# Kernel tuning notes

Measured on AMD Instinct MI355X. Metric: run time of the kernel, lower is better.

## Reference

```python
import jax, jax.numpy as jnp
import numpy as np

B = 8
D = 512        # d_hidn
H = 8          # n_head
DH = 64        # d_head
L = 6          # n_layer
DFF = 2048     # d_ff
GRID = 10
DMLP = 1024
NOUT = 1
EPS = 1e-6
CIN = 2048
SEQ = 1 + 24 * 32 + 9 * 12 + 5 * 7  # 912


def setup_inputs() -> dict:
    key = jax.random.key(0)
    ks = jax.random.split(key, 40)
    rn = lambda k, s, sc=0.02: jax.random.normal(k, s, jnp.float32) * sc
    inp = {
        "feat_dis_org": jax.random.normal(ks[0], (B, CIN, 24, 32), jnp.float32),
        "feat_dis_ref_1": jax.random.normal(ks[1], (B, CIN, 9, 12), jnp.float32),
        "feat_dis_ref_2": jax.random.normal(ks[2], (B, CIN, 5, 7), jnp.float32),
        "conv_w": rn(ks[3], (D, CIN)),
        "conv_b": rn(ks[4], (D,)),
        "scale_org_emb": jax.random.uniform(ks[5], (D,), jnp.float32),
        "ref_1_emb": jax.random.uniform(ks[6], (D,), jnp.float32),
        "ref_2_emb": rn(ks[7], (D,), 1.0),
        "pos_emb": rn(ks[8], (GRID, GRID, D), 0.02),
        "cls_token": rn(ks[9], (D,), 0.02),
        "Wq": rn(ks[10], (L, D, D)), "bq": rn(ks[11], (L, D)),
        "Wk": rn(ks[12], (L, D, D)), "bk": rn(ks[13], (L, D)),
        "Wv": rn(ks[14], (L, D, D)), "bv": rn(ks[15], (L, D)),
        "Wo": rn(ks[16], (L, D, D)), "bo": rn(ks[17], (L, D)),
        "ln1_g": jnp.ones((L, D), jnp.float32), "ln1_b": jnp.zeros((L, D), jnp.float32),
        "w1": rn(ks[18], (L, DFF, D)), "b1": rn(ks[19], (L, DFF)),
        "w2": rn(ks[20], (L, D, DFF)), "b2": rn(ks[21], (L, D)),
        "ln2_g": jnp.ones((L, D), jnp.float32), "ln2_b": jnp.zeros((L, D), jnp.float32),
        "proj_w1": rn(ks[22], (DMLP, D)),
        "proj_w2": rn(ks[23], (NOUT, DMLP)),
        "mask_inputs": jnp.ones((B, SEQ), jnp.int32),
    }
    return inp


def _ln(x, g, b):
    m = jnp.mean(x, -1, keepdims=True)
    v = jnp.mean((x - m) ** 2, -1, keepdims=True)
    return (x - m) * jax.lax.rsqrt(v + EPS) * g + b


def _embed(feat, chan_emb, conv_w, conv_b, pos_emb):
    # 1x1 conv (conv_enc) as a channel contraction: [b,2048,h,w] -> [b,D,h,w]
    x = jnp.einsum('bchw,dc->bdhw', feat, conv_w) + conv_b[None, :, None, None]
    x = x + chan_emb[None, :, None, None]           # scale/ref embedding
    h, w = x.shape[2], x.shape[3]
    # vectorized version of the nested-loop gather: t_i = int(i/h*Grid)
    ti = (jnp.arange(h) * GRID) // h
    tj = (jnp.arange(w) * GRID) // w
    sp = pos_emb[ti][:, tj]                          # [h,w,D]
    x = x + jnp.transpose(sp, (2, 0, 1))[None]       # [b,D,h,w]
    return jnp.transpose(x.reshape(x.shape[0], D, h * w), (0, 2, 1))  # [b,hw,D]


def reference(feat_dis_org, feat_dis_ref_1, feat_dis_ref_2, conv_w, conv_b,
              scale_org_emb, ref_1_emb, ref_2_emb, pos_emb, cls_token,
              Wq, bq, Wk, bk, Wv, bv, Wo, bo, ln1_g, ln1_b,
              w1, b1, w2, b2, ln2_g, ln2_b, proj_w1, proj_w2, mask_inputs):
    t_org = _embed(feat_dis_org, scale_org_emb, conv_w, conv_b, pos_emb)
    t_r1 = _embed(feat_dis_ref_1, ref_1_emb, conv_w, conv_b, pos_emb)
    t_r2 = _embed(feat_dis_ref_2, ref_2_emb, conv_w, conv_b, pos_emb)
    cls = jnp.broadcast_to(cls_token[None, None, :], (B, 1, D))
    x = jnp.concatenate([cls, t_org, t_r1, t_r2], axis=1)   # [B,SEQ,D]

    pad = (mask_inputs == 0)[:, None, None, :]              # [B,1,1,SEQ]
    scale = 1.0 / (DH ** 0.5)

    for i in range(L):
        s = x.shape[1]
        q = (x @ Wq[i].T + bq[i]).reshape(B, s, H, DH).transpose(0, 2, 1, 3)
        k = (x @ Wk[i].T + bk[i]).reshape(B, s, H, DH).transpose(0, 2, 1, 3)
        v = (x @ Wv[i].T + bv[i]).reshape(B, s, H, DH).transpose(0, 2, 1, 3)
        scores = jnp.einsum('bhqd,bhkd->bhqk', q, k) * scale
        scores = jnp.where(pad, -1e9, scores)
        prob = jax.nn.softmax(scores, axis=-1)
        ctx = jnp.einsum('bhqk,bhkd->bhqd', prob, v)
        ctx = ctx.transpose(0, 2, 1, 3).reshape(B, s, H * DH)
        att = ctx @ Wo[i].T + bo[i]
        x = _ln(x + att, ln1_g[i], ln1_b[i])
        ff = jax.nn.gelu(x @ w1[i].T + b1[i], approximate=False) @ w2[i].T + b2[i]
        x = _ln(x + ff, ln2_g[i], ln2_b[i])

    cls_out = x[:, 0, :]
    hmlp = jax.nn.gelu(cls_out @ proj_w1.T, approximate=False)
    pred = hmlp @ proj_w2.T                                   # [B,1]
    return pred
```

## Files before the change

### kernel.cpp

```cpp
#include <hip/hip_runtime.h>
#include <hip/hip_bf16.h>
#include <math.h>

#define SEQ 912
#define NTOK 911
#define CIN_ 2048
#define NLAYER 6

typedef _Float16 f16x8 __attribute__((ext_vector_type(8)));
typedef _Float16 f16x4 __attribute__((ext_vector_type(4)));
typedef float f32x4 __attribute__((ext_vector_type(4)));

__device__ __forceinline__ float gelu_f(float x) {
    return 0.5f * x * (1.0f + erff(x * 0.70710678118654752f));
}

__device__ __forceinline__ int xcd_swizzle(int orig, int nwg) {
    int q = nwg >> 3, r = nwg & 7;
    int xcd = orig & 7, idx = orig >> 3;
    int base = (xcd < r) ? xcd * (q + 1) : r * (q + 1) + (xcd - r) * q;
    return base + idx;
}

__device__ __forceinline__ void gld16(const _Float16* g, _Float16* l) {
    __builtin_amdgcn_global_load_lds(
        (const __attribute__((address_space(1))) unsigned int*)g,
        (__attribute__((address_space(3))) unsigned int*)l,
        16, 0, 0);
}

__device__ __forceinline__ void stage_tile_g(const _Float16* Ab, const _Float16* Bb,
                                             size_t seg, _Float16* ldsW, int kk) {
    gld16(Ab + kk, ldsW);
    gld16(Ab + seg + kk, ldsW + 2048);
    gld16(Bb + kk, ldsW + 4096);
    gld16(Bb + seg + kk, ldsW + 6144);
}

__device__ __forceinline__ void compute_step_g(const _Float16* sb, int r0, int c0,
                                               int ln15, int quad, f32x4 (&acc)[4][4]) {
    f16x8 a[4], b[4];
#pragma unroll
    for (int i = 0; i < 4; ++i)
        a[i] = *(const f16x8*)&sb[(r0 + i * 16 + ln15) * 32 + quad * 8];
#pragma unroll
    for (int j = 0; j < 4; ++j)
        b[j] = *(const f16x8*)&sb[4096 + (c0 + j * 16 + ln15) * 32 + quad * 8];
#pragma unroll
    for (int i = 0; i < 4; ++i)
#pragma unroll
        for (int j = 0; j < 4; ++j)
            acc[i][j] = __builtin_amdgcn_mfma_f32_16x16x32_f16(a[i], b[j], acc[i][j], 0, 0, 0);
}

template <int ACT, int QKV>
__global__ __launch_bounds__(256) void gemm16(
    const _Float16* __restrict__ A, const _Float16* __restrict__ B,
    const float* __restrict__ bias, _Float16* __restrict__ Cout,
    _Float16* __restrict__ vT, int M, int N, int K, int ldc)
{
    __shared__ __align__(16) _Float16 smem[2 * 8192];
    _Float16* Cs = smem;
    const int t = threadIdx.x;
    const int nbx = N >> 7;
    const int swz = xcd_swizzle(blockIdx.x, gridDim.x);
    const int by = swz / nbx, bx = swz - by * nbx;
    const int m0 = by * 128, n0 = bx * 128;
    const int lane = t & 63, w = t >> 6;
    const int r0 = (w >> 1) * 64, c0 = (w & 1) * 64;
    const int ln15 = lane & 15, quad = lane >> 4;

    f32x4 zero = {0.f, 0.f, 0.f, 0.f};
    f32x4 acc[4][4];
#pragma unroll
    for (int i = 0; i < 4; ++i)
#pragma unroll
        for (int j = 0; j < 4; ++j) acc[i][j] = zero;

    const _Float16* Ab = A + (size_t)(m0 + w * 16 + (lane >> 2)) * K + (lane & 3) * 8;
    const _Float16* Bb = B + (size_t)(n0 + w * 16 + (lane >> 2)) * K + (lane & 3) * 8;
    const size_t seg = (size_t)64 * K;
    _Float16* ldsW = smem + w * 512;

    stage_tile_g(Ab, Bb, seg, ldsW, 0);
    __syncthreads();

    const int nK = K >> 5;
    for (int s = 0; s < nK; s += 2) {
        stage_tile_g(Ab, Bb, seg, ldsW + 8192, (s + 1) << 5);
        compute_step_g(smem, r0, c0, ln15, quad, acc);
        __syncthreads();
        if (s + 2 < nK) stage_tile_g(Ab, Bb, seg, ldsW, (s + 2) << 5);
        compute_step_g(smem + 8192, r0, c0, ln15, quad, acc);
        __syncthreads();
    }

    if (QKV && n0 >= 1024) {
#pragma unroll
        for (int j = 0; j < 4; ++j) {
            int gn = n0 + c0 + j * 16 + ln15;
            float bv = bias[gn];
            int chan = gn - 1024;
            int hh = chan >> 6, d = chan & 63;
#pragma unroll
            for (int i = 0; i < 4; ++i) {
                int gmBase = m0 + r0 + i * 16 + quad * 4;
                int bb = gmBase / 912, s = gmBase - bb * 912;
                f16x4 hv4;
#pragma unroll
                for (int r = 0; r < 4; ++r) hv4[r] = (_Float16)(acc[i][j][r] + bv);
                *(f16x4*)&vT[((size_t)((bb * 8 + hh) * 64 + d)) * 960 + s] = hv4;
            }
        }
    } else {
#pragma unroll
        for (int half = 0; half < 2; ++half) {
            if ((w >> 1) == half) {
#pragma unroll
                for (int j = 0; j < 4; ++j) {
                    float bv = bias[n0 + c0 + j * 16 + ln15];
#pragma unroll
                    for (int i = 0; i < 4; ++i)
#pragma unroll
                        for (int r = 0; r < 4; ++r) {
                            float val = acc[i][j][r] + bv;
                            if (ACT == 1) val = gelu_f(val);
                            Cs[(i * 16 + quad * 4 + r) * 136 + c0 + j * 16 + ln15] = (_Float16)val;
                        }
                }
            }
            __syncthreads();
#pragma unroll
            for (int uu = 0; uu < 4; ++uu) {
                int u = t + uu * 256;
                int lr = u >> 4, ch = (u & 15) * 8;
                int gm = m0 + half * 64 + lr;
                if (gm < M)
                    *(f16x8*)&Cout[(size_t)gm * ldc + n0 + ch] = *(const f16x8*)&Cs[lr * 136 + ch];
            }
            __syncthreads();
        }
    }
}

__device__ __forceinline__ void stage_tile_s(const _Float16* Ab, const _Float16* Bb,
                                             size_t seg, _Float16* ldsW, int kk) {
    gld16(Ab + kk, ldsW);
    gld16(Ab + seg + kk, ldsW + 2048);
    gld16(Bb + kk, ldsW + 4096);
}

__device__ __forceinline__ void compute_step_s(const _Float16* sb, int r0, int c0,
                                               int ln15, int quad, f32x4 (&acc)[4][2]) {
    f16x8 a[4], b[2];
#pragma unroll
    for (int i = 0; i < 4; ++i)
        a[i] = *(const f16x8*)&sb[(r0 + i * 16 + ln15) * 32 + quad * 8];
#pragma unroll
    for (int j = 0; j < 2; ++j)
        b[j] = *(const f16x8*)&sb[4096 + (c0 + j * 16 + ln15) * 32 + quad * 8];
#pragma unroll
    for (int i = 0; i < 4; ++i)
#pragma unroll
        for (int j = 0; j < 2; ++j)
            acc[i][j] = __builtin_amdgcn_mfma_f32_16x16x32_f16(a[i], b[j], acc[i][j], 0, 0, 0);
}

__global__ __launch_bounds__(256) void gemm16_splitk(
    const _Float16* __restrict__ A, const _Float16* __restrict__ B,
    float* __restrict__ part, int M, int N, int K)
{
    __shared__ __align__(16) _Float16 smem[2 * 6144];
    const int t = threadIdx.x;
    const int nbx = N >> 6;
    const int swz = xcd_swizzle(blockIdx.x, gridDim.x);
    const int by = swz / nbx, bx = swz - by * nbx;
    const int m0 = by * 128, n0 = bx * 64;
    const int z = blockIdx.z;
    const int lane = t & 63, w = t >> 6;
    const int r0 = (w >> 1) * 64, c0 = (w & 1) * 32;
    const int ln15 = lane & 15, quad = lane >> 4;
    const int Ks = K >> 1;
    const int kBeg = z * Ks;

    f32x4 zero = {0.f, 0.f, 0.f, 0.f};
    f32x4 acc[4][2];
#pragma unroll
    for (int i = 0; i < 4; ++i)
#pragma unroll
        for (int j = 0; j < 2; ++j) acc[i][j] = zero;

    const _Float16* Ab = A + (size_t)(m0 + w * 16 + (lane >> 2)) * K + kBeg + (lane & 3) * 8;
    const _Float16* Bb = B + (size_t)(n0 + w * 16 + (lane >> 2)) * K + kBeg + (lane & 3) * 8;
    const size_t seg = (size_t)64 * K;
    _Float16* ldsW = smem + w * 512;

    stage_tile_s(Ab, Bb, seg, ldsW, 0);
    __syncthreads();

    const int nK = Ks >> 5;
    for (int s = 0; s < nK; s += 2) {
        stage_tile_s(Ab, Bb, seg, ldsW + 6144, (s + 1) << 5);
        compute_step_s(smem, r0, c0, ln15, quad, acc);
        __syncthreads();
        if (s + 2 < nK) stage_tile_s(Ab, Bb, seg, ldsW, (s + 2) << 5);
        compute_step_s(smem + 6144, r0, c0, ln15, quad, acc);
        __syncthreads();
    }

    float* out = part + (size_t)z * M * N;
#pragma unroll
    for (int j = 0; j < 2; ++j) {
        int gn = n0 + c0 + j * 16 + ln15;
#pragma unroll
        for (int i = 0; i < 4; ++i) {
            int gmBase = m0 + r0 + i * 16 + quad * 4;
#pragma unroll
            for (int r = 0; r < 4; ++r) {
                int gm = gmBase + r;
                if (gm < M) out[(size_t)gm * N + gn] = acc[i][j][r];
            }
        }
    }
}

__global__ __launch_bounds__(256) void cast16_kernel(
    const float* __restrict__ src, _Float16* __restrict__ dst, int n4)
{
    int i = blockIdx.x * 256 + threadIdx.x;
    if (i < n4) {
        float4 v = ((const float4*)src)[i];
        f16x4 h;
        h[0] = (_Float16)v.x; h[1] = (_Float16)v.y;
        h[2] = (_Float16)v.z; h[3] = (_Float16)v.w;
        ((f16x4*)dst)[i] = h;
    }
}

__global__ __launch_bounds__(256) void cast2_kernel(
    const float* __restrict__ s1, _Float16* __restrict__ d1, int n4_1,
    const float* __restrict__ s2, _Float16* __restrict__ d2, int n4_2)
{
    int i = blockIdx.x * 256 + threadIdx.x;
    if (i < n4_1) {
        float4 v = ((const float4*)s1)[i];
        f16x4 h;
        h[0] = (_Float16)v.x; h[1] = (_Float16)v.y;
        h[2] = (_Float16)v.z; h[3] = (_Float16)v.w;
        ((f16x4*)d1)[i] = h;
    } else {
        int j = i - n4_1;
        if (j < n4_2) {
            float4 v = ((const float4*)s2)[j];
            f16x4 h;
            h[0] = (_Float16)v.x; h[1] = (_Float16)v.y;
            h[2] = (_Float16)v.z; h[3] = (_Float16)v.w;
            ((f16x4*)d2)[j] = h;
        }
    }
}

__global__ __launch_bounds__(256) void pack_qkvw_kernel(
    const float* __restrict__ Wq, const float* __restrict__ Wk,
    const float* __restrict__ Wv, _Float16* __restrict__ dst)
{
    int idx = blockIdx.x * 256 + threadIdx.x;
    if (idx >= 6 * 1536 * 128) return;
    int c4 = idx & 127;
    int rc = idx >> 7;
    int r = rc % 1536;
    int l = rc / 1536;
    const float* src = (r < 512) ? Wq : (r < 1024) ? Wk : Wv;
    float4 v = *(const float4*)(src + ((size_t)l * 512 + (r & 511)) * 512 + c4 * 4);
    f16x4 h;
    h[0] = (_Float16)v.x; h[1] = (_Float16)v.y;
    h[2] = (_Float16)v.z; h[3] = (_Float16)v.w;
    *(f16x4*)(dst + ((size_t)l * 1536 + r) * 512 + c4 * 4) = h;
}

__global__ __launch_bounds__(256) void pack_qkvb_kernel(
    const float* __restrict__ bq, const float* __restrict__ bk,
    const float* __restrict__ bv, float* __restrict__ dst)
{
    int idx = blockIdx.x * 256 + threadIdx.x;
    if (idx < 6 * 1536) {
        int r = idx % 1536, l = idx / 1536;
        const float* s = (r < 512) ? bq : (r < 1024) ? bk : bv;
        dst[idx] = s[l * 512 + (r & 511)];
    }
}

__global__ __launch_bounds__(256) void transpose_feat_kernel(
    const float* __restrict__ feat, _Float16* __restrict__ patch, int HW, int tok_off)
{
    __shared__ float tile[32][33];
    const int b = blockIdx.z;
    const int c0 = blockIdx.y * 32;
    const int p0 = blockIdx.x * 32;
    const int tx = threadIdx.x, ty = threadIdx.y;
#pragma unroll
    for (int i = 0; i < 4; ++i) {
        int c = c0 + ty + i * 8;
        int p = p0 + tx;
        tile[ty + i * 8][tx] = (p < HW) ? feat[((size_t)b * CIN_ + c) * HW + p] : 0.f;
    }
    __syncthreads();
#pragma unroll
    for (int i = 0; i < 4; ++i) {
        int p = p0 + ty + i * 8;
        int c = c0 + tx;
        if (p < HW)
            patch[((size_t)(b * NTOK + tok_off + p)) * CIN_ + c] = (_Float16)tile[tx][ty + i * 8];
    }
}

__global__ __launch_bounds__(128) void build_x_red(
    const float* __restrict__ part, const float* __restrict__ conv_b,
    const float* __restrict__ cls_token,
    const float* __restrict__ emb_org, const float* __restrict__ emb_r1,
    const float* __restrict__ emb_r2, const float* __restrict__ pos_emb,
    float* __restrict__ x, _Float16* __restrict__ x16)
{
    const size_t ESTR = (size_t)7288 * 512;
    const int row = blockIdx.x;
    const int b = row / SEQ;
    const int tt = row - b * SEQ;
    const int d4 = threadIdx.x;
    float4 o;
    if (tt == 0) {
        o = ((const float4*)cls_token)[d4];
    } else {
        int tp = tt - 1;
        const float* ce; int hh, ww, p;
        if (tp < 768)      { p = tp;       hh = 24; ww = 32; ce = emb_org; }
        else if (tp < 876) { p = tp - 768; hh = 9;  ww = 12; ce = emb_r1; }
        else               { p = tp - 876; hh = 5;  ww = 7;  ce = emb_r2; }
        int i = p / ww, j = p - i * ww;
        int ti = (i * 10) / hh, tj = (j * 10) / ww;
        size_t prow = (size_t)(b * NTOK + tp) * 512;
        float4 t0 = ((const float4*)(part + prow))[d4];
        float4 t1 = ((const float4*)(part + ESTR + prow))[d4];
        float4 cb = ((const float4*)conv_b)[d4];
        float4 cv = ((const float4*)ce)[d4];
        float4 pv = ((const float4*)(pos_emb + (size_t)(ti * 10 + tj) * 512))[d4];
        o.x = t0.x + t1.x + cb.x + cv.x + pv.x;
        o.y = t0.y + t1.y + cb.y + cv.y + pv.y;
        o.z = t0.z + t1.z + cb.z + cv.z + pv.z;
        o.w = t0.w + t1.w + cb.w + cv.w + pv.w;
    }
    ((float4*)(x + (size_t)row * 512))[d4] = o;
    f16x4 h;
    h[0] = (_Float16)o.x; h[1] = (_Float16)o.y;
    h[2] = (_Float16)o.z; h[3] = (_Float16)o.w;
    ((f16x4*)(x16 + (size_t)row * 512))[d4] = h;
}

__global__ __launch_bounds__(64) void ln_residual_red(
    float* __restrict__ x, _Float16* __restrict__ x16,
    const float* __restrict__ part, const float* __restrict__ bias,
    const float* __restrict__ g, const float* __restrict__ bta)
{
    const size_t LSTR = (size_t)7296 * 512;
    const int row = blockIdx.x;
    const int t = threadIdx.x;
    float4* xr = (float4*)(x + (size_t)row * 512);
    const float4* p0 = (const float4*)(part + (size_t)row * 512);
    const float4* p1 = (const float4*)(part + LSTR + (size_t)row * 512);
    const float4* bb = (const float4*)bias;
    float4 a0 = xr[t], a1 = xr[t + 64];
    float4 q0 = p0[t], q1 = p0[t + 64];
    float4 r0 = p1[t], r1 = p1[t + 64];
    float4 c0 = bb[t], c1 = bb[t + 64];
    a0.x += q0.x + r0.x + c0.x; a0.y += q0.y + r0.y + c0.y;
    a0.z += q0.z + r0.z + c0.z; a0.w += q0.w + r0.w + c0.w;
    a1.x += q1.x + r1.x + c1.x; a1.y += q1.y + r1.y + c1.y;
    a1.z += q1.z + r1.z + c1.z; a1.w += q1.w + r1.w + c1.w;
    float s = a0.x + a0.y + a0.z + a0.w + a1.x + a1.y + a1.z + a1.w;
#pragma unroll
    for (int o = 32; o; o >>= 1) s += __shfl_xor(s, o, 64);
    const float mean = s * (1.f / 512.f);
    float sq = 0.f;
    sq += (a0.x - mean) * (a0.x - mean); sq += (a0.y - mean) * (a0.y - mean);
    sq += (a0.z - mean) * (a0.z - mean); sq += (a0.w - mean) * (a0.w - mean);
    sq += (a1.x - mean) * (a1.x - mean); sq += (a1.y - mean) * (a1.y - mean);
    sq += (a1.z - mean) * (a1.z - mean); sq += (a1.w - mean) * (a1.w - mean);
#pragma unroll
    for (int o = 32; o; o >>= 1) sq += __shfl_xor(sq, o, 64);
    const float rstd = rsqrtf(sq * (1.f / 512.f) + 1e-6f);
    const float4 g0 = ((const float4*)g)[t], g1 = ((const float4*)g)[t + 64];
    const float4 e0 = ((const float4*)bta)[t], e1 = ((const float4*)bta)[t + 64];
    float4 o0, o1;
    o0.x = (a0.x - mean) * rstd * g0.x + e0.x;
    o0.y = (a0.y - mean) * rstd * g0.y + e0.y;
    o0.z = (a0.z - mean) * rstd * g0.z + e0.z;
    o0.w = (a0.w - mean) * rstd * g0.w + e0.w;
    o1.x = (a1.x - mean) * rstd * g1.x + e1.x;
    o1.y = (a1.y - mean) * rstd * g1.y + e1.y;
    o1.z = (a1.z - mean) * rstd * g1.z + e1.z;
    o1.w = (a1.w - mean) * rstd * g1.w + e1.w;
    xr[t] = o0; xr[t + 64] = o1;
    f16x4 h0, h1;
    h0[0] = (_Float16)o0.x; h0[1] = (_Float16)o0.y;
    h0[2] = (_Float16)o0.z; h0[3] = (_Float16)o0.w;
    h1[0] = (_Float16)o1.x; h1[1] = (_Float16)o1.y;
    h1[2] = (_Float16)o1.z; h1[3] = (_Float16)o1.w;
    f16x4* xh = (f16x4*)(x16 + (size_t)row * 512);
    xh[t] = h0; xh[t + 64] = h1;
}

__global__ __launch_bounds__(256) void attn_mfma(
    const _Float16* __restrict__ qk, const _Float16* __restrict__ vT,
    const int* __restrict__ mask, _Float16* __restrict__ ctx)
{
    __shared__ __align__(16) _Float16 Ks[64 * 72];
    __shared__ __align__(16) _Float16 VTs[64 * 72];
    __shared__ __align__(16) _Float16 Pw[4][16 * 72];
    __shared__ float biasS[64];
    const int swz = xcd_swizzle(blockIdx.x, 960);
    const int qt = swz % 15;
    const int hb = swz / 15;
    const int h = hb & 7, b = hb >> 3;
    const int q0 = qt * 64;
    const int t = threadIdx.x;
    const int wave = t >> 6, lane = t & 63;
    const int ln15 = lane & 15, quad = lane >> 4;
    const int qrow = q0 + wave * 16 + ln15;

    f16x8 qf[2];
#pragma unroll
    for (int ks = 0; ks < 2; ++ks) {
        f16x8 z = {0, 0, 0, 0, 0, 0, 0, 0};
        qf[ks] = (qrow < SEQ)
            ? *(const f16x8*)(qk + (size_t)(b * SEQ + qrow) * 1024 + h * 64 + ks * 32 + quad * 8)
            : z;
    }

    f32x4 oacc[4];
    f32x4 zero = {0.f, 0.f, 0.f, 0.f};
#pragma unroll
    for (int dj = 0; dj < 4; ++dj) oacc[dj] = zero;
    float m_i = -1e30f, l_i = 0.f;

    for (int kb = 0; kb < 960; kb += 64) {
#pragma unroll
        for (int i = 0; i < 2; ++i) {
            int u = t + i * 256;
            int r = u >> 3, ch = (u & 7) * 8;
            int kg = kb + r;
            f16x8 kvv = {0, 0, 0, 0, 0, 0, 0, 0};
            if (kg < SEQ) kvv = *(const f16x8*)(qk + (size_t)(b * SEQ + kg) * 1024 + 512 + h * 64 + ch);
            *(f16x8*)&Ks[r * 72 + ch] = kvv;
            f16x8 vv = {0, 0, 0, 0, 0, 0, 0, 0};
            if (kb + ch < SEQ)
                vv = *(const f16x8*)(vT + ((size_t)((b * 8 + h) * 64 + r)) * 960 + kb + ch);
            *(f16x8*)&VTs[r * 72 + ch] = vv;
        }
        if (t < 64) {
            int kg = kb + t;
            biasS[t] = (kg < SEQ) ? (mask[b * SEQ + kg] ? 0.f : -1e9f) : -2e9f;
        }
        __syncthreads();

        f32x4 st[4];
#pragma unroll
        for (int jj = 0; jj < 4; ++jj) st[jj] = zero;
#pragma unroll
        for (int jj = 0; jj < 4; ++jj)
#pragma unroll
            for (int ks = 0; ks < 2; ++ks) {
                f16x8 kf = *(const f16x8*)&Ks[(jj * 16 + ln15) * 72 + ks * 32 + quad * 8];
                st[jj] = __builtin_amdgcn_mfma_f32_16x16x32_f16(kf, qf[ks], st[jj], 0, 0, 0);
            }

        float p[4][4];
        float mloc = -3e38f;
#pragma unroll
        for (int jj = 0; jj < 4; ++jj) {
            f32x4 bfr = *(const f32x4*)&biasS[jj * 16 + quad * 4];
#pragma unroll
            for (int r = 0; r < 4; ++r) {
                float sv = st[jj][r] * 0.125f + bfr[r];
                p[jj][r] = sv;
                mloc = fmaxf(mloc, sv);
            }
        }
        mloc = fmaxf(mloc, __shfl_xor(mloc, 16, 64));
        mloc = fmaxf(mloc, __shfl_xor(mloc, 32, 64));
        float mnew = fmaxf(m_i, mloc);
        float alpha = __expf(m_i - mnew);
        m_i = mnew;
        float sloc = 0.f;
#pragma unroll
        for (int jj = 0; jj < 4; ++jj)
#pragma unroll
            for (int r = 0; r < 4; ++r) {
                p[jj][r] = __expf(p[jj][r] - mnew);
                sloc += p[jj][r];
            }
        sloc += __shfl_xor(sloc, 16, 64);
        sloc += __shfl_xor(sloc, 32, 64);
        l_i = l_i * alpha + sloc;

        float ar[4];
#pragma unroll
        for (int r = 0; r < 4; ++r) ar[r] = __shfl(alpha, quad * 4 + r, 64);
#pragma unroll
        for (int dj = 0; dj < 4; ++dj)
#pragma unroll
            for (int r = 0; r < 4; ++r) oacc[dj][r] *= ar[r];

        _Float16* pw = &Pw[wave][0];
#pragma unroll
        for (int jj = 0; jj < 4; ++jj)
#pragma unroll
            for (int r = 0; r < 4; ++r)
                pw[ln15 * 72 + jj * 16 + quad * 4 + r] = (_Float16)p[jj][r];
        f16x8 pf[2];
#pragma unroll
        for (int ks = 0; ks < 2; ++ks)
            pf[ks] = *(const f16x8*)&pw[ln15 * 72 + ks * 32 + quad * 8];

#pragma unroll
        for (int dj = 0; dj < 4; ++dj)
#pragma unroll
            for (int ks = 0; ks < 2; ++ks) {
                f16x8 vf = *(const f16x8*)&VTs[(dj * 16 + ln15) * 72 + ks * 32 + quad * 8];
                oacc[dj] = __builtin_amdgcn_mfma_f32_16x16x32_f16(pf[ks], vf, oacc[dj], 0, 0, 0);
            }
        __syncthreads();
    }

    float linv[4];
#pragma unroll
    for (int r = 0; r < 4; ++r) linv[r] = 1.f / __shfl(l_i, quad * 4 + r, 64);
#pragma unroll
    for (int dj = 0; dj < 4; ++dj)
#pragma unroll
        for (int r = 0; r < 4; ++r) {
            int row = q0 + wave * 16 + quad * 4 + r;
            if (row < SEQ)
                ctx[(size_t)(b * SEQ + row) * 512 + h * 64 + dj * 16 + ln15] =
                    (_Float16)(oacc[dj][r] * linv[r]);
        }
}

__global__ __launch_bounds__(64) void head1_kernel(
    const float* __restrict__ x, const float* __restrict__ w,
    float* __restrict__ hmlp)
{
    const int n = blockIdx.x & 1023;
    const int b = blockIdx.x >> 10;
    const int t = threadIdx.x;
    const float4* cls = (const float4*)(x + (size_t)b * SEQ * 512);
    const float4* wr = (const float4*)(w + (size_t)n * 512);
    float s = 0.f;
#pragma unroll
    for (int i = 0; i < 2; ++i) {
        float4 a = cls[t + i * 64], c = wr[t + i * 64];
        s += a.x * c.x + a.y * c.y + a.z * c.z + a.w * c.w;
    }
#pragma unroll
    for (int o = 32; o; o >>= 1) s += __shfl_xor(s, o, 64);
    if (t == 0) hmlp[b * 1024 + n] = gelu_f(s);
}

__global__ __launch_bounds__(256) void head2_kernel(
    const float* __restrict__ hmlp, const float* __restrict__ w,
    float* __restrict__ out)
{
    __shared__ float red[4];
    const int b = blockIdx.x;
    const int t = threadIdx.x;
    float s = 0.f;
    for (int i = t; i < 1024; i += 256) s += hmlp[b * 1024 + i] * w[i];
#pragma unroll
    for (int o = 32; o; o >>= 1) s += __shfl_xor(s, o, 64);
    if ((t & 63) == 0) red[t >> 6] = s;
    __syncthreads();
    if (t == 0) out[b] = red[0] + red[1] + red[2] + red[3];
}

extern "C" void kernel_launch(void* const* d_in, const int* in_sizes, int n_in,
                              void* d_out, int out_size, void* d_ws, size_t ws_size,
                              hipStream_t stream)
{
    const float* feat_org = (const float*)d_in[0];
    const float* feat_r1  = (const float*)d_in[1];
    const float* feat_r2  = (const float*)d_in[2];
    const float* conv_w   = (const float*)d_in[3];
    const float* conv_b   = (const float*)d_in[4];
    const float* emb_org  = (const float*)d_in[5];
    const float* emb_r1   = (const float*)d_in[6];
    const float* emb_r2   = (const float*)d_in[7];
    const float* pos_emb  = (const float*)d_in[8];
    const float* cls_tok  = (const float*)d_in[9];
    const float* Wq = (const float*)d_in[10];
    const float* bq = (const float*)d_in[11];
    const float* Wk = (const float*)d_in[12];
    const float* bk = (const float*)d_in[13];
    const float* Wv = (const float*)d_in[14];
    const float* bv = (const float*)d_in[15];
    const float* Wo = (const float*)d_in[16];
    const float* bo = (const float*)d_in[17];
    const float* ln1g = (const float*)d_in[18];
    const float* ln1b = (const float*)d_in[19];
    const float* w1 = (const float*)d_in[20];
    const float* b1 = (const float*)d_in[21];
    const float* w2 = (const float*)d_in[22];
    const float* b2 = (const float*)d_in[23];
    const float* ln2g = (const float*)d_in[24];
    const float* ln2b = (const float*)d_in[25];
    const float* pw1 = (const float*)d_in[26];
    const float* pw2 = (const float*)d_in[27];
    const int*   mask = (const int*)d_in[28];

    char* base = (char*)d_ws;
    _Float16* ffh16 = (_Float16*)base;
    _Float16* patch16 = ffh16;
    base += (size_t)7296 * 2048 * 2;
    float* x = (float*)base; base += (size_t)7296 * 512 * 4;
    _Float16* qk16 = (_Float16*)base; base += (size_t)7296 * 1024 * 2;
    _Float16* vT16 = (_Float16*)base; base += (size_t)8 * 8 * 64 * 960 * 2;
    _Float16* ctx16 = (_Float16*)base; base += (size_t)7296 * 512 * 2;
    _Float16* x16   = (_Float16*)base; base += (size_t)7296 * 512 * 2;
    _Float16* wqkv_all = (_Float16*)base; base += (size_t)6 * 1536 * 512 * 2;
    _Float16* wo_all   = (_Float16*)base; base += (size_t)6 * 512 * 512 * 2;
    _Float16* w1_l16   = (_Float16*)base; base += (size_t)2048 * 512 * 2;
    _Float16* w2_l16   = (_Float16*)base; base += (size_t)512 * 2048 * 2;
    float* bqkv_all = (float*)base; base += 6 * 1536 * 4;
    float* hmlp = (float*)base; base += 8 * 1024 * 4;

    float* partO = (float*)ffh16;
    float* partF = (float*)qk16;
    _Float16* convw16 = x16;

    dim3 tb(32, 8);
    hipLaunchKernelGGL(transpose_feat_kernel, dim3(24, 64, 8), tb, 0, stream,
                       feat_org, patch16, 768, 0);
    hipLaunchKernelGGL(transpose_feat_kernel, dim3(4, 64, 8), tb, 0, stream,
                       feat_r1, patch16, 108, 768);
    hipLaunchKernelGGL(transpose_feat_kernel, dim3(2, 64, 8), tb, 0, stream,
                       feat_r2, patch16, 35, 876);
    hipLaunchKernelGGL(cast16_kernel, dim3(1024), 256, 0, stream,
                       conv_w, convw16, 512 * 2048 / 4);
    hipLaunchKernelGGL(cast16_kernel, dim3(1536), 256, 0, stream,
                       Wo, wo_all, 6 * 512 * 512 / 4);
    hipLaunchKernelGGL(pack_qkvw_kernel, dim3(4608), 256, 0, stream,
                       Wq, Wk, Wv, wqkv_all);
    hipLaunchKernelGGL(pack_qkvb_kernel, dim3(36), 256, 0, stream,
                       bq, bk, bv, bqkv_all);

    hipLaunchKernelGGL(gemm16_splitk, dim3(456, 1, 2), 256, 0, stream,
                       patch16, convw16, partF, 7288, 512, 2048);
    hipLaunchKernelGGL(build_x_red, dim3(7296), 128, 0, stream,
                       partF, conv_b, cls_tok, emb_org, emb_r1, emb_r2, pos_emb, x, x16);

    for (int l = 0; l < NLAYER; ++l) {
        hipLaunchKernelGGL(cast2_kernel, dim3(2048), 256, 0, stream,
                           w1 + (size_t)l * 2048 * 512, w1_l16, 2048 * 512 / 4,
                           w2 + (size_t)l * 512 * 2048, w2_l16, 512 * 2048 / 4);
        hipLaunchKernelGGL((gemm16<0, 1>), dim3(684), 256, 0, stream,
                           x16, wqkv_all + (size_t)l * 1536 * 512, bqkv_all + l * 1536,
                           qk16, vT16, 7296, 1536, 512, 1024);
        hipLaunchKernelGGL(attn_mfma, dim3(960), 256, 0, stream,
                           qk16, vT16, mask, ctx16);
        hipLaunchKernelGGL(gemm16_splitk, dim3(456, 1, 2), 256, 0, stream,
                           ctx16, wo_all + (size_t)l * 512 * 512, partO, 7296, 512, 512);
        hipLaunchKernelGGL(ln_residual_red, dim3(7296), 64, 0, stream,
                           x, x16, partO, bo + l * 512, ln1g + l * 512, ln1b + l * 512);
        hipLaunchKernelGGL((gemm16<1, 0>), dim3(912), 256, 0, stream,
                           x16, w1_l16, b1 + l * 2048,
                           ffh16, (_Float16*)nullptr, 7296, 2048, 512, 2048);
        hipLaunchKernelGGL(gemm16_splitk, dim3(456, 1, 2), 256, 0, stream,
                           ffh16, w2_l16, partF, 7296, 512, 2048);
        hipLaunchKernelGGL(ln_residual_red, dim3(7296), 64, 0, stream,
                           x, x16, partF, b2 + l * 512, ln2g + l * 512, ln2b + l * 512);
    }

    hipLaunchKernelGGL(head1_kernel, dim3(8 * 1024), 64, 0, stream, x, pw1, hmlp);
    hipLaunchKernelGGL(head2_kernel, dim3(8), 256, 0, stream, hmlp, pw2, (float*)d_out);
}
```

Measured before the change: 1.375 ms.

## Deepen GEMM LDS pipeline to four stages with explicit vmcnt waits

Both the main fp16 GEMM and the split-K GEMM move from a double-buffered LDS loop with two full __syncthreads per pair of k-steps to a 4-slot ring that keeps two tiles in flight. Each step uses one s_barrier gated by a partial s_waitcnt vmcnt. The aim is to overlap global-to-LDS loads with MFMA compute more deeply and to cut barrier stalls. The cost is doubled LDS per block, which may lower occupancy. Correctness now depends on the exact count of outstanding vm operations that each stage issues.

```diff
diff --git a/kernel.cpp b/kernel.cpp
--- a/kernel.cpp
+++ b/kernel.cpp
@@ -59,7 +59,7 @@
     const float* __restrict__ bias, _Float16* __restrict__ Cout,
     _Float16* __restrict__ vT, int M, int N, int K, int ldc)
 {
-    __shared__ __align__(16) _Float16 smem[2 * 8192];
+    __shared__ __align__(16) _Float16 smem[4 * 8192];
     _Float16* Cs = smem;
     const int t = threadIdx.x;
     const int nbx = N >> 7;
@@ -82,18 +82,25 @@
     const size_t seg = (size_t)64 * K;
     _Float16* ldsW = smem + w * 512;
 
+    const int nK = K >> 5;
     stage_tile_g(Ab, Bb, seg, ldsW, 0);
-    __syncthreads();
-
-    const int nK = K >> 5;
-    for (int s = 0; s < nK; s += 2) {
-        stage_tile_g(Ab, Bb, seg, ldsW + 8192, (s + 1) << 5);
-        compute_step_g(smem, r0, c0, ln15, quad, acc);
-        __syncthreads();
-        if (s + 2 < nK) stage_tile_g(Ab, Bb, seg, ldsW, (s + 2) << 5);
-        compute_step_g(smem + 8192, r0, c0, ln15, quad, acc);
-        __syncthreads();
-    }
+    stage_tile_g(Ab, Bb, seg, ldsW + 8192, 32);
+
+    for (int s = 0; s < nK - 2; ++s) {
+        stage_tile_g(Ab, Bb, seg, ldsW + ((s + 2) & 3) * 8192, (s + 2) << 5);
+        asm volatile("s_waitcnt vmcnt(8)" ::: "memory");
+        __builtin_amdgcn_s_barrier();
+        __builtin_amdgcn_sched_barrier(0);
+        compute_step_g(smem + (s & 3) * 8192, r0, c0, ln15, quad, acc);
+    }
+    asm volatile("s_waitcnt vmcnt(4)" ::: "memory");
+    __builtin_amdgcn_s_barrier();
+    __builtin_amdgcn_sched_barrier(0);
+    compute_step_g(smem + ((nK - 2) & 3) * 8192, r0, c0, ln15, quad, acc);
+    asm volatile("s_waitcnt vmcnt(0)" ::: "memory");
+    __builtin_amdgcn_s_barrier();
+    __builtin_amdgcn_sched_barrier(0);
+    compute_step_g(smem + ((nK - 1) & 3) * 8192, r0, c0, ln15, quad, acc);
 
     if (QKV && n0 >= 1024) {
 #pragma unroll
@@ -113,6 +120,7 @@
             }
         }
     } else {
+        __syncthreads();
 #pragma unroll
         for (int half = 0; half < 2; ++half) {
             if ((w >> 1) == half) {
@@ -170,7 +178,7 @@
     const _Float16* __restrict__ A, const _Float16* __restrict__ B,
     float* __restrict__ part, int M, int N, int K)
 {
-    __shared__ __align__(16) _Float16 smem[2 * 6144];
+    __shared__ __align__(16) _Float16 smem[4 * 6144];
     const int t = threadIdx.x;
     const int nbx = N >> 6;
     const int swz = xcd_swizzle(blockIdx.x, gridDim.x);
@@ -195,18 +203,25 @@
     const size_t seg = (size_t)64 * K;
     _Float16* ldsW = smem + w * 512;
 
+    const int nK = Ks >> 5;
     stage_tile_s(Ab, Bb, seg, ldsW, 0);
-    __syncthreads();
-
-    const int nK = Ks >> 5;
-    for (int s = 0; s < nK; s += 2) {
-        stage_tile_s(Ab, Bb, seg, ldsW + 6144, (s + 1) << 5);
-        compute_step_s(smem, r0, c0, ln15, quad, acc);
-        __syncthreads();
-        if (s + 2 < nK) stage_tile_s(Ab, Bb, seg, ldsW, (s + 2) << 5);
-        compute_step_s(smem + 6144, r0, c0, ln15, quad, acc);
-        __syncthreads();
-    }
+    stage_tile_s(Ab, Bb, seg, ldsW + 6144, 32);
+
+    for (int s = 0; s < nK - 2; ++s) {
+        stage_tile_s(Ab, Bb, seg, ldsW + ((s + 2) & 3) * 6144, (s + 2) << 5);
+        asm volatile("s_waitcnt vmcnt(6)" ::: "memory");
+        __builtin_amdgcn_s_barrier();
+        __builtin_amdgcn_sched_barrier(0);
+        compute_step_s(smem + (s & 3) * 6144, r0, c0, ln15, quad, acc);
+    }
+    asm volatile("s_waitcnt vmcnt(3)" ::: "memory");
+    __builtin_amdgcn_s_barrier();
+    __builtin_amdgcn_sched_barrier(0);
+    compute_step_s(smem + ((nK - 2) & 3) * 6144, r0, c0, ln15, quad, acc);
+    asm volatile("s_waitcnt vmcnt(0)" ::: "memory");
+    __builtin_amdgcn_s_barrier();
+    __builtin_amdgcn_sched_barrier(0);
+    compute_step_s(smem + ((nK - 1) & 3) * 6144, r0, c0, ln15, quad, acc);
 
     float* out = part + (size_t)z * M * N;
 #pragma unroll
```

Result: slower. 1.413 ms (+2.8%).
